# Optimization experiments

Measured on AMD Instinct MI355X. Metric: run time of the kernel, lower is better.

Reference implementation:

```python
import jax, jax.numpy as jnp
import numpy as np

B, L, E, H, V = 32, 2048, 512, 512, 32000  # batch, encoder_len, tar_emb, hid_dim, vocab


def setup_inputs() -> dict:
    key = jax.random.key(0)
    ks = jax.random.split(key, 16)
    w = lambda k, shape: (jax.random.normal(k, shape, jnp.float32) * 0.05)
    emb = w(ks[0], (V, E)).at[0].set(0.0)  # padding_idx=0
    return {
        "x": jax.random.randint(ks[1], (B,), 0, V),
        "h": jax.random.normal(ks[2], (2, B, H), jnp.float32),
        "encoder_out": jax.random.normal(ks[3], (B, L, 2 * H), jnp.float32),
        "emb": emb,
        "attn_W": w(ks[4], (1, 4 * H + E)),
        "attn_b": jnp.zeros((1,), jnp.float32),
        "W_ih_f": w(ks[5], (3 * H, 2 * H)),
        "W_hh_f": w(ks[6], (3 * H, H)),
        "b_ih_f": jnp.zeros((3 * H,), jnp.float32),
        "b_hh_f": jnp.zeros((3 * H,), jnp.float32),
        "W_ih_b": w(ks[7], (3 * H, 2 * H)),
        "W_hh_b": w(ks[8], (3 * H, H)),
        "b_ih_b": jnp.zeros((3 * H,), jnp.float32),
        "b_hh_b": jnp.zeros((3 * H,), jnp.float32),
        "out_W": w(ks[9], (V, 2 * H)),
        "out_b": jnp.zeros((V,), jnp.float32),
    }


def _gru_cell(x, h, W_ih, W_hh, b_ih, b_hh):
    gi = x @ W_ih.T + b_ih          # [B, 3H]
    gh = h @ W_hh.T + b_hh          # [B, 3H]
    i_r, i_z, i_n = jnp.split(gi, 3, axis=-1)
    h_r, h_z, h_n = jnp.split(gh, 3, axis=-1)
    r = jax.nn.sigmoid(i_r + h_r)
    z = jax.nn.sigmoid(i_z + h_z)
    n = jnp.tanh(i_n + r * h_n)
    return (1.0 - z) * n + z * h


def reference(x, h, encoder_out, emb, attn_W, attn_b,
              W_ih_f, W_hh_f, b_ih_f, b_hh_f,
              W_ih_b, W_hh_b, b_ih_b, b_hh_b,
              out_W, out_b):
    x_emb = emb[x]                                     # [B, E]
    Bsz = encoder_out.shape[0]
    prev_h = jnp.transpose(h, (1, 0, 2)).reshape(Bsz, -1)  # [B, 2H]
    # Vectorized equivalent of the per-timestep concat+Linear loop:
    # split attn weight over the concatenated [x_emb, prev_h, enc_t] segments.
    Wx = attn_W[:, :E]                 # [1, E]
    Wp = attn_W[:, E:E + 2 * H]        # [1, 2H]
    We = attn_W[:, E + 2 * H:]         # [1, 2H]
    base = x_emb @ Wx.T + prev_h @ Wp.T + attn_b       # [B, 1]
    scores = base + jnp.einsum('bld,od->bl', encoder_out, We)  # [B, L]
    # Faithful: original applies softmax over the singleton dim of each [B,1]
    # score -> betas are all ones (zero gradient into scores).
    betas = jax.nn.softmax(scores[..., None], axis=-1)[..., 0]  # [B, L] (== 1)
    attn_weights = jax.nn.softmax(betas, axis=1)                # [B, L]
    c = jnp.einsum('bl,bld->bd', attn_weights, encoder_out)     # [B, 2H]
    # n_layers = 1: relu then one bidirectional GRU step (seq_len == 1)
    c = jax.nn.relu(c)
    h_f = _gru_cell(c, h[0], W_ih_f, W_hh_f, b_ih_f, b_hh_f)
    h_b = _gru_cell(c, h[1], W_ih_b, W_hh_b, b_ih_b, b_hh_b)
    c_out = jnp.concatenate([h_f, h_b], axis=-1)       # [B, 2H]
    h_new = jnp.stack([h_f, h_b], axis=0)              # [2, B, H]
    # Faithful: c[-1] in torch indexes the batch dim of [B,1,2H] -> [1,2H]
    logits = c_out[-1:] @ out_W.T + out_b              # [1, V]
    logp = jax.nn.log_softmax(logits, axis=-1)
    return (logp, h_new, attn_weights)
```

## Files before the change

### kernel.cpp

```cpp
#include <hip/hip_runtime.h>
#include <math.h>


#define NC 32

__global__ __launch_bounds__(256) void k_enc_partial(const float* __restrict__ enc,
                                                     float* __restrict__ partial) {
  const int tid = threadIdx.x;
  const int ch  = blockIdx.x;
  const int b   = blockIdx.y;
  const int rows = 2048 / NC;
  const float4* src = (const float4*)enc + ((size_t)b * 2048 + (size_t)ch * rows) * 256 + tid;
  float4 acc = make_float4(0.f, 0.f, 0.f, 0.f);
#pragma unroll 8
  for (int l = 0; l < rows; ++l) {
    float4 v = src[(size_t)l * 256];
    acc.x += v.x; acc.y += v.y; acc.z += v.z; acc.w += v.w;
  }
  ((float4*)partial)[((size_t)b * NC + ch) * 256 + tid] = acc;
}

__global__ __launch_bounds__(256) void k_c_fill(const float* __restrict__ partial,
                                                float* __restrict__ c,
                                                float* __restrict__ out) {
  const int bid = blockIdx.x;
  if (bid < 128) {
    const int idx = bid * 256 + threadIdx.x;
    const int b = idx >> 10, d = idx & 1023;
    float s = 0.f;
#pragma unroll
    for (int ch = 0; ch < NC; ++ch) s += partial[((size_t)b * NC + ch) * 1024 + d];
    s *= (1.0f / 2048.0f);
    c[idx] = s > 0.f ? s : 0.f;
  } else {
    const int i = (bid - 128) * 256 + threadIdx.x;
    out[64768 + i] = 1.0f / 2048.0f;
  }
}

__global__ __launch_bounds__(256) void k_gru(
    const float* __restrict__ c, const float* __restrict__ h,
    const float* __restrict__ Wih_f, const float* __restrict__ Whh_f,
    const float* __restrict__ bih_f, const float* __restrict__ bhh_f,
    const float* __restrict__ Wih_b, const float* __restrict__ Whh_b,
    const float* __restrict__ bih_b, const float* __restrict__ bhh_b,
    float* __restrict__ out) {
  const int lane = threadIdx.x & 63;
  const int wid  = (blockIdx.x * 256 + threadIdx.x) >> 6;
  const int dir  = wid >> 9;
  const int k    = wid & 511;
  const float* Wih = dir ? Wih_b : Wih_f;
  const float* Whh = dir ? Whh_b : Whh_f;
  const float* bih = dir ? bih_b : bih_f;
  const float* bhh = dir ? bhh_b : bhh_f;
  const float4* Wih4 = (const float4*)Wih;
  const float4* Whh4 = (const float4*)Whh;

  float4 wr[4], wz[4], wn[4];
#pragma unroll
  for (int i = 0; i < 4; ++i) {
    wr[i] = Wih4[(size_t)k * 256 + i * 64 + lane];
    wz[i] = Wih4[(size_t)(k + 512) * 256 + i * 64 + lane];
    wn[i] = Wih4[(size_t)(k + 1024) * 256 + i * 64 + lane];
  }
  float4 ur[2], uz[2], un[2];
#pragma unroll
  for (int i = 0; i < 2; ++i) {
    ur[i] = Whh4[(size_t)k * 128 + i * 64 + lane];
    uz[i] = Whh4[(size_t)(k + 512) * 128 + i * 64 + lane];
    un[i] = Whh4[(size_t)(k + 1024) * 128 + i * 64 + lane];
  }
  const float bkr = bih[k], bkz = bih[k + 512], bkn = bih[k + 1024];
  const float ckr = bhh[k], ckz = bhh[k + 512], ckn = bhh[k + 1024];

  const float4* c4 = (const float4*)c;
  const float4* h4 = (const float4*)h + (size_t)dir * 32 * 128;

  for (int b = 0; b < 32; ++b) {
    float pr = 0.f, pz = 0.f, pn = 0.f;
#pragma unroll
    for (int i = 0; i < 4; ++i) {
      float4 v = c4[b * 256 + i * 64 + lane];
      pr += v.x * wr[i].x + v.y * wr[i].y + v.z * wr[i].z + v.w * wr[i].w;
      pz += v.x * wz[i].x + v.y * wz[i].y + v.z * wz[i].z + v.w * wz[i].w;
      pn += v.x * wn[i].x + v.y * wn[i].y + v.z * wn[i].z + v.w * wn[i].w;
    }
    float qr = 0.f, qz = 0.f, qn = 0.f;
#pragma unroll
    for (int i = 0; i < 2; ++i) {
      float4 v = h4[b * 128 + i * 64 + lane];
      qr += v.x * ur[i].x + v.y * ur[i].y + v.z * ur[i].z + v.w * ur[i].w;
      qz += v.x * uz[i].x + v.y * uz[i].y + v.z * uz[i].z + v.w * uz[i].w;
      qn += v.x * un[i].x + v.y * un[i].y + v.z * un[i].z + v.w * un[i].w;
    }
#pragma unroll
    for (int off = 32; off; off >>= 1) {
      pr += __shfl_xor(pr, off, 64);
      pz += __shfl_xor(pz, off, 64);
      pn += __shfl_xor(pn, off, 64);
      qr += __shfl_xor(qr, off, 64);
      qz += __shfl_xor(qz, off, 64);
      qn += __shfl_xor(qn, off, 64);
    }
    if (lane == 0) {
      float r = 1.f / (1.f + expf(-(pr + bkr + qr + ckr)));
      float z = 1.f / (1.f + expf(-(pz + bkz + qz + ckz)));
      float n = tanhf(pn + bkn + r * (qn + ckn));
      float hp = h[(size_t)dir * 32 * 512 + (size_t)b * 512 + k];
      out[32000 + dir * 16384 + b * 512 + k] = (1.f - z) * n + z * hp;
    }
  }
}

__global__ __launch_bounds__(256) void k_logits(const float* __restrict__ outW,
                                                const float* __restrict__ outb,
                                                const float* __restrict__ dout,
                                                float* __restrict__ logits) {
  const int lane = threadIdx.x & 63;
  const int v = (blockIdx.x * 256 + threadIdx.x) >> 6;
  const float4* hf = (const float4*)(dout + 32000 + 31 * 512);
  const float4* hb = (const float4*)(dout + 32000 + 16384 + 31 * 512);
  const float4* W4 = (const float4*)outW + (size_t)v * 256;
  float p = 0.f;
#pragma unroll
  for (int i = 0; i < 4; ++i) {
    const int pos = i * 64 + lane;
    float4 cv = (pos < 128) ? hf[pos] : hb[pos - 128];
    float4 wv = W4[pos];
    p += cv.x * wv.x + cv.y * wv.y + cv.z * wv.z + cv.w * wv.w;
  }
#pragma unroll
  for (int off = 32; off; off >>= 1) p += __shfl_xor(p, off, 64);
  if (lane == 0) logits[v] = p + outb[v];
}

__global__ __launch_bounds__(1024) void k_lse_logp(const float* __restrict__ logits,
                                                   float* __restrict__ out) {
  __shared__ float red[16];
  __shared__ float s_m, s_ls;
  const int tid = threadIdx.x, lane = tid & 63, w = tid >> 6;
  float m = -1e30f;
  for (int i = tid; i < 32000; i += 1024) m = fmaxf(m, logits[i]);
#pragma unroll
  for (int off = 32; off; off >>= 1) m = fmaxf(m, __shfl_xor(m, off, 64));
  if (lane == 0) red[w] = m;
  __syncthreads();
  if (tid == 0) {
    float mm = red[0];
    for (int i = 1; i < 16; ++i) mm = fmaxf(mm, red[i]);
    s_m = mm;
  }
  __syncthreads();
  const float gm = s_m;
  float s = 0.f;
  for (int i = tid; i < 32000; i += 1024) s += expf(logits[i] - gm);
#pragma unroll
  for (int off = 32; off; off >>= 1) s += __shfl_xor(s, off, 64);
  if (lane == 0) red[w] = s;
  __syncthreads();
  if (tid == 0) {
    float ss = 0.f;
    for (int i = 0; i < 16; ++i) ss += red[i];
    s_ls = logf(ss);
  }
  __syncthreads();
  const float sub = gm + s_ls;
  for (int i = tid; i < 32000; i += 1024) out[i] = logits[i] - sub;
}

extern "C" void kernel_launch(void* const* d_in, const int* in_sizes, int n_in,
                              void* d_out, int out_size, void* d_ws, size_t ws_size,
                              hipStream_t stream) {
  const float* h     = (const float*)d_in[1];
  const float* enc   = (const float*)d_in[2];
  const float* Wih_f = (const float*)d_in[6];
  const float* Whh_f = (const float*)d_in[7];
  const float* bih_f = (const float*)d_in[8];
  const float* bhh_f = (const float*)d_in[9];
  const float* Wih_b = (const float*)d_in[10];
  const float* Whh_b = (const float*)d_in[11];
  const float* bih_b = (const float*)d_in[12];
  const float* bhh_b = (const float*)d_in[13];
  const float* outW  = (const float*)d_in[14];
  const float* outb  = (const float*)d_in[15];
  float* out = (float*)d_out;
  float* ws  = (float*)d_ws;

  float* partial = ws;
  float* cbuf    = partial + 32 * NC * 1024;
  float* logits  = cbuf + 32768;

  dim3 g1(NC, 32);
  k_enc_partial<<<g1, 256, 0, stream>>>(enc, partial);
  k_c_fill<<<384, 256, 0, stream>>>(partial, cbuf, out);
  k_gru<<<256, 256, 0, stream>>>(cbuf, h, Wih_f, Whh_f, bih_f, bhh_f,
                                 Wih_b, Whh_b, bih_b, bhh_b, out);
  k_logits<<<8000, 256, 0, stream>>>(outW, outb, out, logits);
  k_lse_logp<<<1, 1024, 0, stream>>>(logits, out);
}
```

Measured before the change: 541.3 us.

## Fuse all stages into one cooperative persistent kernel with grid syncs

Replaces the five-kernel pipeline with a single cooperative kernel of 256 blocks that runs encoder reduction, c computation, GRU, logits and log-softmax in phases separated by grid.sync, and keeps the old kernels as a fallback if the cooperative launch fails. This removes launch gaps between stages, but the encoder sum (the dominant 256MB stream) now runs on only 256 blocks × 256 threads instead of 1024 blocks. That reduced parallelism and memory-level concurrency on a bandwidth-bound read is a serious risk. The logits phase also loops with fewer waves.

After: 818.9 us. 51.3% more time.

```diff
diff --git a/kernel.cpp b/kernel.cpp
--- a/kernel.cpp
+++ b/kernel.cpp
@@ -1,6 +1,185 @@
 #include <hip/hip_runtime.h>
+#include <hip/hip_cooperative_groups.h>
 #include <math.h>
 
+namespace cg = cooperative_groups;
+
+
+struct Params {
+  const float* h;
+  const float* enc;
+  const float* Wih_f; const float* Whh_f; const float* bih_f; const float* bhh_f;
+  const float* Wih_b; const float* Whh_b; const float* bih_b; const float* bhh_b;
+  const float* outW; const float* outb;
+  float* out;
+  float* partial;
+  float* cbuf;
+  float* logits;
+};
+
+__global__ __launch_bounds__(256, 2) void mega(Params p) {
+  cg::grid_group grid = cg::this_grid();
+  const int tid  = threadIdx.x;
+  const int bid  = blockIdx.x;
+  const int lane = tid & 63;
+
+  {
+    const int b  = bid >> 3;
+    const int ch = bid & 7;
+    const float4* src = (const float4*)p.enc + ((size_t)b * 2048 + ch * 256) * 256 + tid;
+    float4 acc = make_float4(0.f, 0.f, 0.f, 0.f);
+#pragma unroll 8
+    for (int l = 0; l < 256; ++l) {
+      float4 v = src[(size_t)l * 256];
+      acc.x += v.x; acc.y += v.y; acc.z += v.z; acc.w += v.w;
+    }
+    ((float4*)p.partial)[(size_t)bid * 256 + tid] = acc;
+  }
+  __threadfence();
+  grid.sync();
+
+  if (bid < 128) {
+    const int idx = bid * 256 + tid;
+    const int b = idx >> 10, d = idx & 1023;
+    float s = 0.f;
+#pragma unroll
+    for (int ch = 0; ch < 8; ++ch) s += p.partial[(size_t)(b * 8 + ch) * 1024 + d];
+    s *= (1.0f / 2048.0f);
+    p.cbuf[idx] = s > 0.f ? s : 0.f;
+  } else {
+    const int i = (bid - 128) * 256 + tid;
+    p.out[64768 + i] = 1.0f / 2048.0f;
+    p.out[64768 + 32768 + i] = 1.0f / 2048.0f;
+  }
+  __threadfence();
+  grid.sync();
+
+  {
+    const int w   = bid * 4 + (tid >> 6);
+    const int dir = w >> 9;
+    const int k   = w & 511;
+    const float* Wih = dir ? p.Wih_b : p.Wih_f;
+    const float* Whh = dir ? p.Whh_b : p.Whh_f;
+    const float* bih = dir ? p.bih_b : p.bih_f;
+    const float* bhh = dir ? p.bhh_b : p.bhh_f;
+    const float4* Wih4 = (const float4*)Wih;
+    const float4* Whh4 = (const float4*)Whh;
+
+    float4 wr[4], wz[4], wn[4];
+#pragma unroll
+    for (int i = 0; i < 4; ++i) {
+      wr[i] = Wih4[(size_t)k * 256 + i * 64 + lane];
+      wz[i] = Wih4[(size_t)(k + 512) * 256 + i * 64 + lane];
+      wn[i] = Wih4[(size_t)(k + 1024) * 256 + i * 64 + lane];
+    }
+    float4 ur[2], uz[2], un[2];
+#pragma unroll
+    for (int i = 0; i < 2; ++i) {
+      ur[i] = Whh4[(size_t)k * 128 + i * 64 + lane];
+      uz[i] = Whh4[(size_t)(k + 512) * 128 + i * 64 + lane];
+      un[i] = Whh4[(size_t)(k + 1024) * 128 + i * 64 + lane];
+    }
+    const float bkr = bih[k], bkz = bih[k + 512], bkn = bih[k + 1024];
+    const float ckr = bhh[k], ckz = bhh[k + 512], ckn = bhh[k + 1024];
+
+    const float4* c4 = (const float4*)p.cbuf;
+    const float4* h4 = (const float4*)p.h + (size_t)dir * 32 * 128;
+
+    for (int b = 0; b < 32; ++b) {
+      float pr = 0.f, pz = 0.f, pn = 0.f;
+#pragma unroll
+      for (int i = 0; i < 4; ++i) {
+        float4 v = c4[b * 256 + i * 64 + lane];
+        pr += v.x * wr[i].x + v.y * wr[i].y + v.z * wr[i].z + v.w * wr[i].w;
+        pz += v.x * wz[i].x + v.y * wz[i].y + v.z * wz[i].z + v.w * wz[i].w;
+        pn += v.x * wn[i].x + v.y * wn[i].y + v.z * wn[i].z + v.w * wn[i].w;
+      }
+      float qr = 0.f, qz = 0.f, qn = 0.f;
+#pragma unroll
+      for (int i = 0; i < 2; ++i) {
+        float4 v = h4[b * 128 + i * 64 + lane];
+        qr += v.x * ur[i].x + v.y * ur[i].y + v.z * ur[i].z + v.w * ur[i].w;
+        qz += v.x * uz[i].x + v.y * uz[i].y + v.z * uz[i].z + v.w * uz[i].w;
+        qn += v.x * un[i].x + v.y * un[i].y + v.z * un[i].z + v.w * un[i].w;
+      }
+#pragma unroll
+      for (int off = 32; off; off >>= 1) {
+        pr += __shfl_xor(pr, off, 64);
+        pz += __shfl_xor(pz, off, 64);
+        pn += __shfl_xor(pn, off, 64);
+        qr += __shfl_xor(qr, off, 64);
+        qz += __shfl_xor(qz, off, 64);
+        qn += __shfl_xor(qn, off, 64);
+      }
+      if (lane == 0) {
+        float r = 1.f / (1.f + expf(-(pr + bkr + qr + ckr)));
+        float z = 1.f / (1.f + expf(-(pz + bkz + qz + ckz)));
+        float n = tanhf(pn + bkn + r * (qn + ckn));
+        float hp = p.h[(size_t)dir * 32 * 512 + (size_t)b * 512 + k];
+        p.out[32000 + dir * 16384 + b * 512 + k] = (1.f - z) * n + z * hp;
+      }
+    }
+  }
+  __threadfence();
+  grid.sync();
+
+  {
+    const int w = bid * 4 + (tid >> 6);
+    const float4* hf = (const float4*)(p.out + 32000 + 31 * 512);
+    const float4* hb = (const float4*)(p.out + 32000 + 16384 + 31 * 512);
+    float4 cv[4];
+#pragma unroll
+    for (int i = 0; i < 4; ++i) {
+      const int pos = i * 64 + lane;
+      cv[i] = (pos < 128) ? hf[pos] : hb[pos - 128];
+    }
+    for (int v = w; v < 32000; v += 1024) {
+      const float4* W4 = (const float4*)p.outW + (size_t)v * 256;
+      float acc = 0.f;
+#pragma unroll
+      for (int i = 0; i < 4; ++i) {
+        float4 wv = W4[i * 64 + lane];
+        acc += cv[i].x * wv.x + cv[i].y * wv.y + cv[i].z * wv.z + cv[i].w * wv.w;
+      }
+#pragma unroll
+      for (int off = 32; off; off >>= 1) acc += __shfl_xor(acc, off, 64);
+      if (lane == 0) p.logits[v] = acc + p.outb[v];
+    }
+  }
+  __threadfence();
+  grid.sync();
+
+  if (bid == 0) {
+    __shared__ float red[4];
+    const float4* l4 = (const float4*)p.logits;
+    float m = -1e30f;
+    for (int i = tid; i < 8000; i += 256) {
+      float4 v = l4[i];
+      m = fmaxf(m, fmaxf(fmaxf(v.x, v.y), fmaxf(v.z, v.w)));
+    }
+#pragma unroll
+    for (int off = 32; off; off >>= 1) m = fmaxf(m, __shfl_xor(m, off, 64));
+    if (lane == 0) red[tid >> 6] = m;
+    __syncthreads();
+    const float gm = fmaxf(fmaxf(red[0], red[1]), fmaxf(red[2], red[3]));
+    __syncthreads();
+    float s = 0.f;
+    for (int i = tid; i < 8000; i += 256) {
+      float4 v = l4[i];
+      s += expf(v.x - gm) + expf(v.y - gm) + expf(v.z - gm) + expf(v.w - gm);
+    }
+#pragma unroll
+    for (int off = 32; off; off >>= 1) s += __shfl_xor(s, off, 64);
+    if (lane == 0) red[tid >> 6] = s;
+    __syncthreads();
+    const float sub = gm + logf(red[0] + red[1] + red[2] + red[3]);
+    float4* o4 = (float4*)p.out;
+    for (int i = tid; i < 8000; i += 256) {
+      float4 v = l4[i];
+      o4[i] = make_float4(v.x - sub, v.y - sub, v.z - sub, v.w - sub);
+    }
+  }
+}
 
 #define NC 32
 
@@ -171,30 +350,35 @@
 extern "C" void kernel_launch(void* const* d_in, const int* in_sizes, int n_in,
                               void* d_out, int out_size, void* d_ws, size_t ws_size,
                               hipStream_t stream) {
-  const float* h     = (const float*)d_in[1];
-  const float* enc   = (const float*)d_in[2];
-  const float* Wih_f = (const float*)d_in[6];
-  const float* Whh_f = (const float*)d_in[7];
-  const float* bih_f = (const float*)d_in[8];
-  const float* bhh_f = (const float*)d_in[9];
-  const float* Wih_b = (const float*)d_in[10];
-  const float* Whh_b = (const float*)d_in[11];
-  const float* bih_b = (const float*)d_in[12];
-  const float* bhh_b = (const float*)d_in[13];
-  const float* outW  = (const float*)d_in[14];
-  const float* outb  = (const float*)d_in[15];
-  float* out = (float*)d_out;
-  float* ws  = (float*)d_ws;
-
-  float* partial = ws;
-  float* cbuf    = partial + 32 * NC * 1024;
-  float* logits  = cbuf + 32768;
-
-  dim3 g1(NC, 32);
-  k_enc_partial<<<g1, 256, 0, stream>>>(enc, partial);
-  k_c_fill<<<384, 256, 0, stream>>>(partial, cbuf, out);
-  k_gru<<<256, 256, 0, stream>>>(cbuf, h, Wih_f, Whh_f, bih_f, bhh_f,
-                                 Wih_b, Whh_b, bih_b, bhh_b, out);
-  k_logits<<<8000, 256, 0, stream>>>(outW, outb, out, logits);
-  k_lse_logp<<<1, 1024, 0, stream>>>(logits, out);
-}
+  float* ws = (float*)d_ws;
+  Params p;
+  p.h     = (const float*)d_in[1];
+  p.enc   = (const float*)d_in[2];
+  p.Wih_f = (const float*)d_in[6];
+  p.Whh_f = (const float*)d_in[7];
+  p.bih_f = (const float*)d_in[8];
+  p.bhh_f = (const float*)d_in[9];
+  p.Wih_b = (const float*)d_in[10];
+  p.Whh_b = (const float*)d_in[11];
+  p.bih_b = (const float*)d_in[12];
+  p.bhh_b = (const float*)d_in[13];
+  p.outW  = (const float*)d_in[14];
+  p.outb  = (const float*)d_in[15];
+  p.out   = (float*)d_out;
+  p.partial = ws;
+  p.cbuf    = ws + 32 * 32 * 1024;
+  p.logits  = p.cbuf + 32768;
+
+  void* args[] = { &p };
+  hipError_t err = hipLaunchCooperativeKernel(reinterpret_cast<void*>(&mega),
+                                              dim3(256), dim3(256), args, 0, stream);
+  if (err != hipSuccess) {
+    dim3 g1(NC, 32);
+    k_enc_partial<<<g1, 256, 0, stream>>>(p.enc, p.partial);
+    k_c_fill<<<384, 256, 0, stream>>>(p.partial, p.cbuf, p.out);
+    k_gru<<<256, 256, 0, stream>>>(p.cbuf, p.h, p.Wih_f, p.Whh_f, p.bih_f, p.bhh_f,
+                                   p.Wih_b, p.Whh_b, p.bih_b, p.bhh_b, p.out);
+    k_logits<<<8000, 256, 0, stream>>>(p.outW, p.outb, p.out, p.logits);
+    k_lse_logp<<<1, 1024, 0, stream>>>(p.logits, p.out);
+  }
+}
```
